# Kernel tuning notes

Measured on AMD Instinct MI355X. Metric: run time of the kernel, lower is better.

## Reference

```python
import jax, jax.numpy as jnp
import numpy as np

D_MODEL = 1024
N_HEADS = 16
D_HEAD = D_MODEL // N_HEADS
BSZ, SEQ = 1, 4096


def setup_inputs() -> dict:
    key = jax.random.key(0)
    ks = jax.random.split(key, 7)
    scale = 1.0 / np.sqrt(D_MODEL)
    q = jax.random.normal(ks[0], (BSZ, SEQ, D_MODEL), dtype=jnp.float32)
    k = jax.random.normal(ks[1], (BSZ, SEQ, D_MODEL), dtype=jnp.float32)
    v = jax.random.normal(ks[2], (BSZ, SEQ, D_MODEL), dtype=jnp.float32)
    Wq = jax.random.normal(ks[3], (D_MODEL, D_MODEL), dtype=jnp.float32) * scale
    Wk = jax.random.normal(ks[4], (D_MODEL, D_MODEL), dtype=jnp.float32) * scale
    Wv = jax.random.normal(ks[5], (D_MODEL, D_MODEL), dtype=jnp.float32) * scale
    Wo = jax.random.normal(ks[6], (D_MODEL, D_MODEL), dtype=jnp.float32) * scale
    # causal mask: 1 = attend, 0 = masked (matches torch masked_fill(mask == 0, -inf))
    mask = jnp.tril(jnp.ones((SEQ, SEQ), dtype=jnp.int32))[None, None, :, :]
    return {"q": q, "k": k, "v": v, "mask": mask, "Wq": Wq, "Wk": Wk, "Wv": Wv, "Wo": Wo}


def reference(q, k, v, mask, Wq, Wk, Wv, Wo):
    bsz, seq, _ = q.shape
    # nn.Linear(d,d,bias=False): y = x @ W.T
    Q = (q @ Wq.T).reshape(bsz, seq, N_HEADS, D_HEAD).transpose(0, 2, 1, 3)
    K = (k @ Wk.T).reshape(bsz, seq, N_HEADS, D_HEAD).transpose(0, 2, 1, 3)
    V = (v @ Wv.T).reshape(bsz, seq, N_HEADS, D_HEAD).transpose(0, 2, 1, 3)
    scores = jnp.einsum("bhqd,bhkd->bhqk", Q, K) / np.sqrt(D_HEAD).astype(np.float32)
    scores = jnp.where(mask == 0, -jnp.inf, scores)
    attn = jax.nn.softmax(scores, axis=-1)
    out = jnp.einsum("bhqk,bhkd->bhqd", attn, V)
    out = out.transpose(0, 2, 1, 3).reshape(bsz, seq, D_MODEL)
    return out @ Wo.T
```

## Files before the change

kernel.cpp:

```cpp
#include <hip/hip_runtime.h>


typedef __attribute__((ext_vector_type(8))) short bf16x8;
typedef __attribute__((ext_vector_type(4))) float f32x4;
typedef __attribute__((ext_vector_type(16))) float f32x16;

#define S_LEN 4096
#define DM 1024
#define NH 16
#define DH 64

static __device__ __forceinline__ unsigned short f2bf(float f) {
  union { float f; unsigned u; } x; x.f = f;
  unsigned u = x.u;
  u += 0x7fffu + ((u >> 16) & 1u);
  return (unsigned short)(u >> 16);
}

static __device__ __forceinline__ unsigned pk2(float lo, float hi) {
  unsigned r;
  asm("v_cvt_pk_bf16_f32 %0, %1, %2" : "=v"(r) : "v"(lo), "v"(hi));
  return r;
}

static __device__ __forceinline__ float exp2_(float x) {
#if __has_builtin(__builtin_amdgcn_exp2f)
  return __builtin_amdgcn_exp2f(x);
#else
  return exp2f(x);
#endif
}

#define GLL16(gsrc, ldst)                                                      \
  __builtin_amdgcn_global_load_lds(                                            \
      (const __attribute__((address_space(1))) void*)(gsrc),                   \
      (__attribute__((address_space(3))) void*)(ldst), 16, 0, 0)

struct CastArgs {
  const float* src[8];
  unsigned short* dst[8];
  int n[8];
  float scl[8];
};

__global__ __launch_bounds__(256) void cast_all(CastArgs a) {
  int which = blockIdx.y;
  const float* __restrict__ src = a.src[which];
  unsigned short* __restrict__ dst = a.dst[which];
  int n = a.n[which];
  float s = a.scl[which];
  int i = (blockIdx.x * 256 + threadIdx.x) * 8;
  if (i >= n) return;
  f32x4 v0 = *(const f32x4*)(src + i);
  f32x4 v1 = *(const f32x4*)(src + i + 4);
  union { bf16x8 v; unsigned short u[8]; } o;
#pragma unroll
  for (int j = 0; j < 4; j++) { o.u[j] = f2bf(v0[j] * s); o.u[4 + j] = f2bf(v1[j] * s); }
  *(bf16x8*)(dst + i) = o.v;
}

static __device__ __forceinline__ void gemm_body(
    const unsigned short* __restrict__ A, const unsigned short* __restrict__ B,
    void* __restrict__ Cout, int mode, unsigned short* As, unsigned short* Bs) {
  const int K = 1024;
  int tid = threadIdx.x;
  int wid = tid >> 6, lane = tid & 63;
  int m0 = blockIdx.y * 128, n0 = blockIdx.x * 128;
  int wr = (wid >> 1) * 64, wc = (wid & 1) * 64;
  int g = lane >> 4, r = lane & 15;

  int lin = wid * 1024 + lane * 16;
  int row0 = lin >> 6;
  int el0 = (lin & 63) >> 1;
  const unsigned short* gA0 = A + (size_t)(m0 + row0) * K + el0;
  const unsigned short* gA1 = gA0 + (size_t)64 * K;
  const unsigned short* gB0 = B + (size_t)(n0 + row0) * K + el0;
  const unsigned short* gB1 = gB0 + (size_t)64 * K;
  unsigned short* lA = As + wid * 512;
  unsigned short* lB = Bs + wid * 512;

  f32x4 acc[4][4] = {};

  for (int k0 = 0; k0 < K; k0 += 32) {
    GLL16(gA0 + k0, lA);
    GLL16(gA1 + k0, lA + 2048);
    GLL16(gB0 + k0, lB);
    GLL16(gB1 + k0, lB + 2048);
    __syncthreads();

    bf16x8 af[4], bfr[4];
#pragma unroll
    for (int mi = 0; mi < 4; mi++)
      af[mi] = *(const bf16x8*)&As[(wr + mi * 16 + r) * 32 + g * 8];
#pragma unroll
    for (int ni = 0; ni < 4; ni++)
      bfr[ni] = *(const bf16x8*)&Bs[(wc + ni * 16 + r) * 32 + g * 8];
#pragma unroll
    for (int mi = 0; mi < 4; mi++)
#pragma unroll
      for (int ni = 0; ni < 4; ni++)
        acc[mi][ni] = __builtin_amdgcn_mfma_f32_16x16x32_bf16(
            af[mi], bfr[ni], acc[mi][ni], 0, 0, 0);
    __syncthreads();
  }

  if (mode == 0) {
    float* C = (float*)Cout;
#pragma unroll
    for (int mi = 0; mi < 4; mi++) {
      int row = m0 + wr + mi * 16 + g * 4;
#pragma unroll
      for (int ni = 0; ni < 4; ni++) {
        int c = n0 + wc + ni * 16 + r;
#pragma unroll
        for (int j = 0; j < 4; j++)
          C[(size_t)(row + j) * DM + c] = acc[mi][ni][j];
      }
    }
  } else if (mode == 1) {
    unsigned short* Cb = (unsigned short*)Cout;
#pragma unroll
    for (int mi = 0; mi < 4; mi++) {
      int row = m0 + wr + mi * 16 + g * 4;
#pragma unroll
      for (int ni = 0; ni < 4; ni++) {
        int c = n0 + wc + ni * 16 + r;
        int h = c >> 6, d = c & 63;
#pragma unroll
        for (int j = 0; j < 4; j++)
          Cb[(size_t)h * (S_LEN * DH) + (size_t)(row + j) * DH + d] =
              f2bf(acc[mi][ni][j]);
      }
    }
  } else {
    unsigned short* Cb = (unsigned short*)Cout;
#pragma unroll
    for (int mi = 0; mi < 4; mi++) {
      int row = m0 + wr + mi * 16 + g * 4;
#pragma unroll
      for (int ni = 0; ni < 4; ni++) {
        int c = n0 + wc + ni * 16 + r;
        int h = c >> 6, d = c & 63;
#pragma unroll
        for (int j = 0; j < 4; j++)
          Cb[(size_t)h * (S_LEN * DH) + (size_t)d * S_LEN + (row + j)] =
              f2bf(acc[mi][ni][j]);
      }
    }
  }
}

struct ProjArgs {
  const unsigned short* A[3];
  const unsigned short* B[3];
  unsigned short* C[3];
  int mode[3];
};

__global__ __launch_bounds__(256, 2) void gemm_proj(ProjArgs p) {
  __shared__ unsigned short As[4096];
  __shared__ unsigned short Bs[4096];
  int z = blockIdx.z;
  gemm_body(p.A[z], p.B[z], p.C[z], p.mode[z], As, Bs);
}

__global__ __launch_bounds__(256, 2) void gemm_one(
    const unsigned short* __restrict__ A, const unsigned short* __restrict__ B,
    void* __restrict__ Cout, int mode) {
  __shared__ unsigned short As[4096];
  __shared__ unsigned short Bs[4096];
  gemm_body(A, B, Cout, mode, As, Bs);
}

__global__ __launch_bounds__(512, 4) void attn_fwd(
    const unsigned short* __restrict__ Qh, const unsigned short* __restrict__ Kh,
    const unsigned short* __restrict__ Vt, unsigned short* __restrict__ O) {
  __shared__ char smem[65536];

  const int b = blockIdx.x;
  const int hd = b & 15;
  const int t = b >> 4;
  const int qe = (t < 16) ? (31 - 2 * t) : (2 * (t - 16));
  const int q0 = qe * 128;
  const int nt = qe + 1;

  const int tid = threadIdx.x;
  const int gg = tid >> 8;
  const int ww = (tid >> 6) & 3;
  const int lane = tid & 63;
  const int l31 = lane & 31, hi = lane >> 5;
  const int qi = ww;
  const int qw = q0 + qi * 32;
  const int qrow = qw + l31;
  const int sw = (l31 & 7) << 4;

  const unsigned short* Qb = Qh + (size_t)hd * (S_LEN * DH);
  const char* Kb = (const char*)(Kh + (size_t)hd * (S_LEN * DH));
  const char* Vb = (const char*)(Vt + (size_t)hd * (S_LEN * DH));

  bf16x8 qf[4];
#pragma unroll
  for (int m = 0; m < 4; m++)
    qf[m] = *(const bf16x8*)&Qb[(size_t)qrow * DH + m * 16 + hi * 8];

  const int roleV = (ww >= 2);
  const int wv = ww & 1;
  const char* gb = roleV ? Vb : Kb;
  const long tstep = roleV ? 128 : 8192;
  int soff[4];
#pragma unroll
  for (int q2 = 0; q2 < 4; q2++) {
    int rowl = wv * 32 + q2 * 8 + (lane >> 3);
    int cb = ((lane & 7) * 16) ^ (((lane >> 3) & 7) << 4);
    soff[q2] = roleV ? (rowl * 8192 + cb) : (rowl * 128 + cb);
  }
  const int ldsc = gg * 32768 + roleV * 8192 + wv * 4096;

  f32x16 oacc[2] = {};
  float m_r = -1e30f, l_r = 0.f;

  {
    const char* gp = gb + (long)(gg * nt) * tstep;
#pragma unroll
    for (int q2 = 0; q2 < 4; q2++)
      GLL16(gp + soff[q2], smem + ldsc + q2 * 1024);
  }
  __syncthreads();

  int db = 0;
  for (int it = 0; it < nt; ++it) {
    if (it + 1 < nt) {
      const char* gp = gb + (long)(gg * nt + it + 1) * tstep;
      char* lb = smem + ldsc + (db ^ 1) * 16384;
#pragma unroll
      for (int q2 = 0; q2 < 4; q2++)
        GLL16(gp + soff[q2], lb + q2 * 1024);
    }
    const int kv0 = (gg * nt + it) * 64;
    const char* Kc = smem + gg * 32768 + db * 16384;
    const char* Vc = Kc + 8192;

    if (kv0 <= qw + 31) {
      const bool hiP = (kv0 + 32 <= qw + 31);
      const bool interior = (kv0 + 63 <= qw);
      f32x16 s0 = {}, s1 = {};
#pragma unroll
      for (int m = 0; m < 4; m++) {
        bf16x8 kf = *(const bf16x8*)(Kc + l31 * 128 + ((m * 32 + hi * 16) ^ sw));
        s0 = __builtin_amdgcn_mfma_f32_32x32x16_bf16(kf, qf[m], s0, 0, 0, 0);
      }
      if (hiP) {
#pragma unroll
        for (int m = 0; m < 4; m++) {
          bf16x8 kf = *(const bf16x8*)(Kc + (32 + l31) * 128 + ((m * 32 + hi * 16) ^ sw));
          s1 = __builtin_amdgcn_mfma_f32_32x32x16_bf16(kf, qf[m], s1, 0, 0, 0);
        }
      }
      if (!interior) {
#pragma unroll
        for (int rg = 0; rg < 16; rg++) {
          const int kvl = (rg & 3) + 8 * (rg >> 2) + 4 * hi;
          s0[rg] = (kv0 + kvl <= qrow) ? s0[rg] : -1e30f;
          s1[rg] = (hiP && kv0 + 32 + kvl <= qrow) ? s1[rg] : -1e30f;
        }
      }
      float a0 = fmaxf(s0[0], s0[1]),  a1 = fmaxf(s0[2], s0[3]);
      float a2 = fmaxf(s0[4], s0[5]),  a3 = fmaxf(s0[6], s0[7]);
      float a4 = fmaxf(s0[8], s0[9]),  a5 = fmaxf(s0[10], s0[11]);
      float a6 = fmaxf(s0[12], s0[13]), a7 = fmaxf(s0[14], s0[15]);
      float b0 = fmaxf(s1[0], s1[1]),  b1 = fmaxf(s1[2], s1[3]);
      float b2 = fmaxf(s1[4], s1[5]),  b3 = fmaxf(s1[6], s1[7]);
      float b4 = fmaxf(s1[8], s1[9]),  b5 = fmaxf(s1[10], s1[11]);
      float b6 = fmaxf(s1[12], s1[13]), b7 = fmaxf(s1[14], s1[15]);
      float c0 = fmaxf(fmaxf(a0, a1), fmaxf(a2, a3));
      float c1 = fmaxf(fmaxf(a4, a5), fmaxf(a6, a7));
      float c2 = fmaxf(fmaxf(b0, b1), fmaxf(b2, b3));
      float c3 = fmaxf(fmaxf(b4, b5), fmaxf(b6, b7));
      float mx = fmaxf(fmaxf(c0, c1), fmaxf(c2, c3));
      mx = fmaxf(mx, __shfl_xor(mx, 32, 64));
      if (__any(mx > m_r + 10.0f)) {
        float mnew = fmaxf(m_r, mx);
        float sc = exp2_(m_r - mnew);
        m_r = mnew;
        l_r *= sc;
#pragma unroll
        for (int dt = 0; dt < 2; dt++)
#pragma unroll
          for (int rg = 0; rg < 16; rg++) oacc[dt][rg] *= sc;
      }
#pragma unroll
      for (int rg = 0; rg < 16; rg++) {
        s0[rg] = exp2_(s0[rg] - m_r);
        s1[rg] = exp2_(s1[rg] - m_r);
      }
      float r0 = (s0[0] + s0[1]) + (s0[2] + s0[3]);
      float r1 = (s0[4] + s0[5]) + (s0[6] + s0[7]);
      float r2 = (s0[8] + s0[9]) + (s0[10] + s0[11]);
      float r3 = (s0[12] + s0[13]) + (s0[14] + s0[15]);
      float r4 = (s1[0] + s1[1]) + (s1[2] + s1[3]);
      float r5 = (s1[4] + s1[5]) + (s1[6] + s1[7]);
      float r6 = (s1[8] + s1[9]) + (s1[10] + s1[11]);
      float r7 = (s1[12] + s1[13]) + (s1[14] + s1[15]);
      float rs = ((r0 + r1) + (r2 + r3)) + ((r4 + r5) + (r6 + r7));
      rs += __shfl_xor(rs, 32, 64);
      l_r += rs;
#pragma unroll
      for (int c = 0; c < 2; c++) {
        if (c == 0 || hiP) {
          const f32x16 P = c ? s1 : s0;
          uint2 pk[4], pp[4];
#pragma unroll
          for (int blk = 0; blk < 4; blk++) {
            pk[blk].x = pk2(P[blk * 4 + 0], P[blk * 4 + 1]);
            pk[blk].y = pk2(P[blk * 4 + 2], P[blk * 4 + 3]);
            pp[blk].x = (unsigned)__shfl_xor((int)pk[blk].x, 32, 64);
            pp[blk].y = (unsigned)__shfl_xor((int)pk[blk].y, 32, 64);
          }
#pragma unroll
          for (int n = 0; n < 2; n++) {
            union { unsigned w[4]; bf16x8 v; } u;
            u.w[0] = hi ? pp[2 * n + 1].x : pk[2 * n].x;
            u.w[1] = hi ? pp[2 * n + 1].y : pk[2 * n].y;
            u.w[2] = hi ? pk[2 * n + 1].x : pp[2 * n].x;
            u.w[3] = hi ? pk[2 * n + 1].y : pp[2 * n].y;
#pragma unroll
            for (int dt = 0; dt < 2; dt++) {
              bf16x8 vf = *(const bf16x8*)(Vc + (dt * 32 + l31) * 128 +
                            ((c * 64 + n * 32 + hi * 16) ^ sw));
              oacc[dt] = __builtin_amdgcn_mfma_f32_32x32x16_bf16(
                  vf, u.v, oacc[dt], 0, 0, 0);
            }
          }
        }
      }
    }
    __syncthreads();
    db ^= 1;
  }

  float* scr = (float*)smem;
  const int sbase = (qi * 64 + lane) * 35;
  if (gg == 1) {
#pragma unroll
    for (int dt = 0; dt < 2; dt++)
#pragma unroll
      for (int rg = 0; rg < 16; rg++) scr[sbase + dt * 16 + rg] = oacc[dt][rg];
    scr[sbase + 32] = m_r;
    scr[sbase + 33] = l_r;
  }
  __syncthreads();
  if (gg == 0) {
    float mB = scr[sbase + 32], lB = scr[sbase + 33];
    float mS = fmaxf(m_r, mB);
    float sA = exp2_(m_r - mS);
    float sB = exp2_(mB - mS);
    float rl = 1.0f / (l_r * sA + lB * sB);
    float fA = sA * rl, fB = sB * rl;
#pragma unroll
    for (int dt = 0; dt < 2; dt++)
#pragma unroll
      for (int blk = 0; blk < 4; blk++) {
        float v0 = oacc[dt][blk * 4 + 0] * fA + scr[sbase + dt * 16 + blk * 4 + 0] * fB;
        float v1 = oacc[dt][blk * 4 + 1] * fA + scr[sbase + dt * 16 + blk * 4 + 1] * fB;
        float v2 = oacc[dt][blk * 4 + 2] * fA + scr[sbase + dt * 16 + blk * 4 + 2] * fB;
        float v3 = oacc[dt][blk * 4 + 3] * fA + scr[sbase + dt * 16 + blk * 4 + 3] * fB;
        uint2 st; st.x = pk2(v0, v1); st.y = pk2(v2, v3);
        int d0 = dt * 32 + blk * 8 + 4 * hi;
        *(uint2*)&O[(size_t)qrow * DM + hd * DH + d0] = st;
      }
  }
}

extern "C" void kernel_launch(void* const* d_in, const int* in_sizes, int n_in,
                              void* d_out, int out_size, void* d_ws, size_t ws_size,
                              hipStream_t stream) {
  const float* q = (const float*)d_in[0];
  const float* k = (const float*)d_in[1];
  const float* v = (const float*)d_in[2];
  const float* Wq = (const float*)d_in[4];
  const float* Wk = (const float*)d_in[5];
  const float* Wv = (const float*)d_in[6];
  const float* Wo = (const float*)d_in[7];

  unsigned short* W = (unsigned short*)d_ws;
  const int SM = S_LEN * DM;
  const int WM = DM * DM;
  unsigned short* qb  = W;
  unsigned short* kb  = qb + SM;
  unsigned short* vb  = kb + SM;
  unsigned short* Wqb = vb + SM;
  unsigned short* Wkb = Wqb + WM;
  unsigned short* Wvb = Wkb + WM;
  unsigned short* Wob = Wvb + WM;
  unsigned short* Qh  = Wob + WM;
  unsigned short* Kh  = Qh + SM;
  unsigned short* Vt  = Kh + SM;
  unsigned short* Ob  = Vt + SM;

  CastArgs ca;
  ca.src[0] = q;  ca.dst[0] = qb;  ca.n[0] = SM; ca.scl[0] = 1.f;
  ca.src[1] = k;  ca.dst[1] = kb;  ca.n[1] = SM; ca.scl[1] = 1.f;
  ca.src[2] = v;  ca.dst[2] = vb;  ca.n[2] = SM; ca.scl[2] = 1.f;
  ca.src[3] = Wq; ca.dst[3] = Wqb; ca.n[3] = WM; ca.scl[3] = 0.125f * 1.44269504f;
  ca.src[4] = Wk; ca.dst[4] = Wkb; ca.n[4] = WM; ca.scl[4] = 1.f;
  ca.src[5] = Wv; ca.dst[5] = Wvb; ca.n[5] = WM; ca.scl[5] = 1.f;
  ca.src[6] = Wo; ca.dst[6] = Wob; ca.n[6] = WM; ca.scl[6] = 1.f;
  ca.src[7] = Wo; ca.dst[7] = Wob; ca.n[7] = 0;  ca.scl[7] = 1.f;
  cast_all<<<dim3(2048, 8), 256, 0, stream>>>(ca);

  ProjArgs pa;
  pa.A[0] = qb; pa.B[0] = Wqb; pa.C[0] = Qh; pa.mode[0] = 1;
  pa.A[1] = kb; pa.B[1] = Wkb; pa.C[1] = Kh; pa.mode[1] = 1;
  pa.A[2] = vb; pa.B[2] = Wvb; pa.C[2] = Vt; pa.mode[2] = 2;
  gemm_proj<<<dim3(8, 32, 3), 256, 0, stream>>>(pa);

  attn_fwd<<<dim3(512), 512, 0, stream>>>(Qh, Kh, Vt, Ob);

  gemm_one<<<dim3(8, 32), 256, 0, stream>>>(Ob, Wob, d_out, 0);
}
```

Before: 142.6 us.

## Restructure attention to direct-global 32-row strips and widen GEMM K tile with swizzle

The attention kernel drops its LDS double-buffered K/V staging. Each block now handles one 32-query strip with two waves splitting the KV range, loading K and a new tiled V layout straight from global memory into registers, and raising MFMA priority with setprio. The V projection output is rewritten into 64x64 tiles to match. The GEMM doubles its K step to 64 and adds an XOR swizzle in LDS to reduce bank conflicts and halve barrier count. The aim is to remove LDS traffic, barriers and the coarse 128-row causal imbalance, at the cost of relying on L2 for K/V reuse across blocks.

```diff
diff --git a/kernel.cpp b/kernel.cpp
--- a/kernel.cpp
+++ b/kernel.cpp
@@ -69,38 +69,43 @@
   int wr = (wid >> 1) * 64, wc = (wid & 1) * 64;
   int g = lane >> 4, r = lane & 15;
 
-  int lin = wid * 1024 + lane * 16;
-  int row0 = lin >> 6;
-  int el0 = (lin & 63) >> 1;
-  const unsigned short* gA0 = A + (size_t)(m0 + row0) * K + el0;
-  const unsigned short* gA1 = gA0 + (size_t)64 * K;
-  const unsigned short* gB0 = B + (size_t)(n0 + row0) * K + el0;
-  const unsigned short* gB1 = gB0 + (size_t)64 * K;
-  unsigned short* lA = As + wid * 512;
-  unsigned short* lB = Bs + wid * 512;
+  const int srow = wid * 8 + (lane >> 3);
+  const int scol = 8 * ((lane & 7) ^ ((lane >> 3) & 7));
+  const unsigned short* gA[4];
+  const unsigned short* gB[4];
+#pragma unroll
+  for (int rr = 0; rr < 4; rr++) {
+    gA[rr] = A + (size_t)(m0 + rr * 32 + srow) * K + scol;
+    gB[rr] = B + (size_t)(n0 + rr * 32 + srow) * K + scol;
+  }
 
   f32x4 acc[4][4] = {};
-
-  for (int k0 = 0; k0 < K; k0 += 32) {
-    GLL16(gA0 + k0, lA);
-    GLL16(gA1 + k0, lA + 2048);
-    GLL16(gB0 + k0, lB);
-    GLL16(gB1 + k0, lB + 2048);
+  const int rsw = (r & 7) << 3;
+
+  for (int k0 = 0; k0 < K; k0 += 64) {
+#pragma unroll
+    for (int rr = 0; rr < 4; rr++) {
+      GLL16(gA[rr] + k0, As + wid * 512 + rr * 2048);
+      GLL16(gB[rr] + k0, Bs + wid * 512 + rr * 2048);
+    }
     __syncthreads();
 
-    bf16x8 af[4], bfr[4];
-#pragma unroll
-    for (int mi = 0; mi < 4; mi++)
-      af[mi] = *(const bf16x8*)&As[(wr + mi * 16 + r) * 32 + g * 8];
-#pragma unroll
-    for (int ni = 0; ni < 4; ni++)
-      bfr[ni] = *(const bf16x8*)&Bs[(wc + ni * 16 + r) * 32 + g * 8];
-#pragma unroll
-    for (int mi = 0; mi < 4; mi++)
+#pragma unroll
+    for (int kk = 0; kk < 64; kk += 32) {
+      bf16x8 af[4], bfr[4];
+#pragma unroll
+      for (int mi = 0; mi < 4; mi++)
+        af[mi] = *(const bf16x8*)&As[(wr + mi * 16 + r) * 64 + ((kk + g * 8) ^ rsw)];
 #pragma unroll
       for (int ni = 0; ni < 4; ni++)
-        acc[mi][ni] = __builtin_amdgcn_mfma_f32_16x16x32_bf16(
-            af[mi], bfr[ni], acc[mi][ni], 0, 0, 0);
+        bfr[ni] = *(const bf16x8*)&Bs[(wc + ni * 16 + r) * 64 + ((kk + g * 8) ^ rsw)];
+#pragma unroll
+      for (int mi = 0; mi < 4; mi++)
+#pragma unroll
+        for (int ni = 0; ni < 4; ni++)
+          acc[mi][ni] = __builtin_amdgcn_mfma_f32_16x16x32_bf16(
+              af[mi], bfr[ni], acc[mi][ni], 0, 0, 0);
+    }
     __syncthreads();
   }
 
@@ -142,9 +147,11 @@
         int c = n0 + wc + ni * 16 + r;
         int h = c >> 6, d = c & 63;
 #pragma unroll
-        for (int j = 0; j < 4; j++)
-          Cb[(size_t)h * (S_LEN * DH) + (size_t)d * S_LEN + (row + j)] =
+        for (int j = 0; j < 4; j++) {
+          int s = row + j;
+          Cb[(size_t)h * (S_LEN * DH) + (size_t)(s >> 6) * 4096 + d * 64 + (s & 63)] =
               f2bf(acc[mi][ni][j]);
+        }
       }
     }
   }
@@ -158,8 +165,8 @@
 };
 
 __global__ __launch_bounds__(256, 2) void gemm_proj(ProjArgs p) {
-  __shared__ unsigned short As[4096];
-  __shared__ unsigned short Bs[4096];
+  __shared__ unsigned short As[8192];
+  __shared__ unsigned short Bs[8192];
   int z = blockIdx.z;
   gemm_body(p.A[z], p.B[z], p.C[z], p.mode[z], As, Bs);
 }
@@ -167,179 +174,152 @@
 __global__ __launch_bounds__(256, 2) void gemm_one(
     const unsigned short* __restrict__ A, const unsigned short* __restrict__ B,
     void* __restrict__ Cout, int mode) {
-  __shared__ unsigned short As[4096];
-  __shared__ unsigned short Bs[4096];
+  __shared__ unsigned short As[8192];
+  __shared__ unsigned short Bs[8192];
   gemm_body(A, B, Cout, mode, As, Bs);
 }
 
-__global__ __launch_bounds__(512, 4) void attn_fwd(
+__global__ __launch_bounds__(128, 3) void attn_fwd(
     const unsigned short* __restrict__ Qh, const unsigned short* __restrict__ Kh,
-    const unsigned short* __restrict__ Vt, unsigned short* __restrict__ O) {
-  __shared__ char smem[65536];
+    const unsigned short* __restrict__ V4, unsigned short* __restrict__ O) {
+  __shared__ float scr[64 * 35];
 
   const int b = blockIdx.x;
   const int hd = b & 15;
-  const int t = b >> 4;
-  const int qe = (t < 16) ? (31 - 2 * t) : (2 * (t - 16));
-  const int q0 = qe * 128;
-  const int nt = qe + 1;
-
+  const int u = b >> 4;
+  const int strip = (u < 64) ? (127 - 2 * u) : (2 * (u - 64));
+  const int qw = strip * 32;
   const int tid = threadIdx.x;
-  const int gg = tid >> 8;
-  const int ww = (tid >> 6) & 3;
+  const int gg = tid >> 6;
   const int lane = tid & 63;
   const int l31 = lane & 31, hi = lane >> 5;
-  const int qi = ww;
-  const int qw = q0 + qi * 32;
   const int qrow = qw + l31;
-  const int sw = (l31 & 7) << 4;
 
   const unsigned short* Qb = Qh + (size_t)hd * (S_LEN * DH);
-  const char* Kb = (const char*)(Kh + (size_t)hd * (S_LEN * DH));
-  const char* Vb = (const char*)(Vt + (size_t)hd * (S_LEN * DH));
+  const unsigned short* Kb = Kh + (size_t)hd * (S_LEN * DH);
+  const unsigned short* Vb = V4 + (size_t)hd * (S_LEN * DH);
 
   bf16x8 qf[4];
 #pragma unroll
   for (int m = 0; m < 4; m++)
     qf[m] = *(const bf16x8*)&Qb[(size_t)qrow * DH + m * 16 + hi * 8];
 
-  const int roleV = (ww >= 2);
-  const int wv = ww & 1;
-  const char* gb = roleV ? Vb : Kb;
-  const long tstep = roleV ? 128 : 8192;
-  int soff[4];
-#pragma unroll
-  for (int q2 = 0; q2 < 4; q2++) {
-    int rowl = wv * 32 + q2 * 8 + (lane >> 3);
-    int cb = ((lane & 7) * 16) ^ (((lane >> 3) & 7) << 4);
-    soff[q2] = roleV ? (rowl * 8192 + cb) : (rowl * 128 + cb);
-  }
-  const int ldsc = gg * 32768 + roleV * 8192 + wv * 4096;
-
   f32x16 oacc[2] = {};
   float m_r = -1e30f, l_r = 0.f;
 
-  {
-    const char* gp = gb + (long)(gg * nt) * tstep;
-#pragma unroll
-    for (int q2 = 0; q2 < 4; q2++)
-      GLL16(gp + soff[q2], smem + ldsc + q2 * 1024);
-  }
-  __syncthreads();
-
-  int db = 0;
-  for (int it = 0; it < nt; ++it) {
-    if (it + 1 < nt) {
-      const char* gp = gb + (long)(gg * nt + it + 1) * tstep;
-      char* lb = smem + ldsc + (db ^ 1) * 16384;
-#pragma unroll
-      for (int q2 = 0; q2 < 4; q2++)
-        GLL16(gp + soff[q2], lb + q2 * 1024);
-    }
-    const int kv0 = (gg * nt + it) * 64;
-    const char* Kc = smem + gg * 32768 + db * 16384;
-    const char* Vc = Kc + 8192;
-
-    if (kv0 <= qw + 31) {
-      const bool hiP = (kv0 + 32 <= qw + 31);
-      const bool interior = (kv0 + 63 <= qw);
-      f32x16 s0 = {}, s1 = {};
-#pragma unroll
-      for (int m = 0; m < 4; m++) {
-        bf16x8 kf = *(const bf16x8*)(Kc + l31 * 128 + ((m * 32 + hi * 16) ^ sw));
-        s0 = __builtin_amdgcn_mfma_f32_32x32x16_bf16(kf, qf[m], s0, 0, 0, 0);
-      }
-      if (hiP) {
-#pragma unroll
-        for (int m = 0; m < 4; m++) {
-          bf16x8 kf = *(const bf16x8*)(Kc + (32 + l31) * 128 + ((m * 32 + hi * 16) ^ sw));
-          s1 = __builtin_amdgcn_mfma_f32_32x32x16_bf16(kf, qf[m], s1, 0, 0, 0);
-        }
-      }
-      if (!interior) {
-#pragma unroll
-        for (int rg = 0; rg < 16; rg++) {
-          const int kvl = (rg & 3) + 8 * (rg >> 2) + 4 * hi;
-          s0[rg] = (kv0 + kvl <= qrow) ? s0[rg] : -1e30f;
-          s1[rg] = (hiP && kv0 + 32 + kvl <= qrow) ? s1[rg] : -1e30f;
-        }
-      }
-      float a0 = fmaxf(s0[0], s0[1]),  a1 = fmaxf(s0[2], s0[3]);
-      float a2 = fmaxf(s0[4], s0[5]),  a3 = fmaxf(s0[6], s0[7]);
-      float a4 = fmaxf(s0[8], s0[9]),  a5 = fmaxf(s0[10], s0[11]);
-      float a6 = fmaxf(s0[12], s0[13]), a7 = fmaxf(s0[14], s0[15]);
-      float b0 = fmaxf(s1[0], s1[1]),  b1 = fmaxf(s1[2], s1[3]);
-      float b2 = fmaxf(s1[4], s1[5]),  b3 = fmaxf(s1[6], s1[7]);
-      float b4 = fmaxf(s1[8], s1[9]),  b5 = fmaxf(s1[10], s1[11]);
-      float b6 = fmaxf(s1[12], s1[13]), b7 = fmaxf(s1[14], s1[15]);
-      float c0 = fmaxf(fmaxf(a0, a1), fmaxf(a2, a3));
-      float c1 = fmaxf(fmaxf(a4, a5), fmaxf(a6, a7));
-      float c2 = fmaxf(fmaxf(b0, b1), fmaxf(b2, b3));
-      float c3 = fmaxf(fmaxf(b4, b5), fmaxf(b6, b7));
-      float mx = fmaxf(fmaxf(c0, c1), fmaxf(c2, c3));
-      mx = fmaxf(mx, __shfl_xor(mx, 32, 64));
-      if (__any(mx > m_r + 10.0f)) {
-        float mnew = fmaxf(m_r, mx);
-        float sc = exp2_(m_r - mnew);
-        m_r = mnew;
-        l_r *= sc;
+  const int nt = (strip >> 1) + 1;
+  const int nh = nt >> 1;
+  const int tb = gg ? nh : 0;
+  const int te = gg ? nt : nh;
+
+  for (int t = tb; t < te; ++t) {
+    const int kv0 = t * 64;
+    const bool hiP = (kv0 + 32 <= qw + 31);
+    const bool diag = (kv0 + 63 > qw);
+    const unsigned short* Kt = Kb + (size_t)kv0 * DH;
+    const unsigned short* Vt = Vb + (size_t)t * 4096;
+
+    bf16x8 kf0[4], kf1[4];
+#pragma unroll
+    for (int m = 0; m < 4; m++)
+      kf0[m] = *(const bf16x8*)&Kt[l31 * DH + m * 16 + hi * 8];
+#pragma unroll
+    for (int m = 0; m < 4; m++)
+      kf1[m] = *(const bf16x8*)&Kt[(32 + l31) * DH + m * 16 + hi * 8];
+    bf16x8 vf[8];
+#pragma unroll
+    for (int i = 0; i < 8; i++) {
+      const int dt = i >> 2, c = (i >> 1) & 1, n = i & 1;
+      vf[i] = *(const bf16x8*)&Vt[(dt * 32 + l31) * 64 + c * 32 + n * 16 + hi * 8];
+    }
+
+    f32x16 s0 = {}, s1 = {};
+    __builtin_amdgcn_s_setprio(1);
+#pragma unroll
+    for (int m = 0; m < 4; m++)
+      s0 = __builtin_amdgcn_mfma_f32_32x32x16_bf16(kf0[m], qf[m], s0, 0, 0, 0);
+#pragma unroll
+    for (int m = 0; m < 4; m++)
+      s1 = __builtin_amdgcn_mfma_f32_32x32x16_bf16(kf1[m], qf[m], s1, 0, 0, 0);
+    __builtin_amdgcn_s_setprio(0);
+
+    if (diag) {
+#pragma unroll
+      for (int rg = 0; rg < 16; rg++) {
+        const int kvl = (rg & 3) + 8 * (rg >> 2) + 4 * hi;
+        s0[rg] = (kv0 + kvl <= qrow) ? s0[rg] : -1e30f;
+        s1[rg] = (hiP && kv0 + 32 + kvl <= qrow) ? s1[rg] : -1e30f;
+      }
+    }
+    float a0 = fmaxf(s0[0], s0[1]),  a1 = fmaxf(s0[2], s0[3]);
+    float a2 = fmaxf(s0[4], s0[5]),  a3 = fmaxf(s0[6], s0[7]);
+    float a4 = fmaxf(s0[8], s0[9]),  a5 = fmaxf(s0[10], s0[11]);
+    float a6 = fmaxf(s0[12], s0[13]), a7 = fmaxf(s0[14], s0[15]);
+    float b0 = fmaxf(s1[0], s1[1]),  b1 = fmaxf(s1[2], s1[3]);
+    float b2 = fmaxf(s1[4], s1[5]),  b3 = fmaxf(s1[6], s1[7]);
+    float b4 = fmaxf(s1[8], s1[9]),  b5 = fmaxf(s1[10], s1[11]);
+    float b6 = fmaxf(s1[12], s1[13]), b7 = fmaxf(s1[14], s1[15]);
+    float c0 = fmaxf(fmaxf(a0, a1), fmaxf(a2, a3));
+    float c1 = fmaxf(fmaxf(a4, a5), fmaxf(a6, a7));
+    float c2 = fmaxf(fmaxf(b0, b1), fmaxf(b2, b3));
+    float c3 = fmaxf(fmaxf(b4, b5), fmaxf(b6, b7));
+    float mx = fmaxf(fmaxf(c0, c1), fmaxf(c2, c3));
+    mx = fmaxf(mx, __shfl_xor(mx, 32, 64));
+    if (__any(mx > m_r + 10.0f)) {
+      float mnew = fmaxf(m_r, mx);
+      float sc = exp2_(m_r - mnew);
+      m_r = mnew;
+      l_r *= sc;
+#pragma unroll
+      for (int dt = 0; dt < 2; dt++)
+#pragma unroll
+        for (int rg = 0; rg < 16; rg++) oacc[dt][rg] *= sc;
+    }
+#pragma unroll
+    for (int rg = 0; rg < 16; rg++) {
+      s0[rg] = exp2_(s0[rg] - m_r);
+      s1[rg] = exp2_(s1[rg] - m_r);
+    }
+    float r0 = (s0[0] + s0[1]) + (s0[2] + s0[3]);
+    float r1 = (s0[4] + s0[5]) + (s0[6] + s0[7]);
+    float r2 = (s0[8] + s0[9]) + (s0[10] + s0[11]);
+    float r3 = (s0[12] + s0[13]) + (s0[14] + s0[15]);
+    float r4 = (s1[0] + s1[1]) + (s1[2] + s1[3]);
+    float r5 = (s1[4] + s1[5]) + (s1[6] + s1[7]);
+    float r6 = (s1[8] + s1[9]) + (s1[10] + s1[11]);
+    float r7 = (s1[12] + s1[13]) + (s1[14] + s1[15]);
+    float rs = ((r0 + r1) + (r2 + r3)) + ((r4 + r5) + (r6 + r7));
+    rs += __shfl_xor(rs, 32, 64);
+    l_r += rs;
+#pragma unroll
+    for (int c = 0; c < 2; c++) {
+      const f32x16 P = c ? s1 : s0;
+      uint2 pk[4], pp[4];
+#pragma unroll
+      for (int blk = 0; blk < 4; blk++) {
+        pk[blk].x = pk2(P[blk * 4 + 0], P[blk * 4 + 1]);
+        pk[blk].y = pk2(P[blk * 4 + 2], P[blk * 4 + 3]);
+        pp[blk].x = (unsigned)__shfl_xor((int)pk[blk].x, 32, 64);
+        pp[blk].y = (unsigned)__shfl_xor((int)pk[blk].y, 32, 64);
+      }
+      __builtin_amdgcn_s_setprio(1);
+#pragma unroll
+      for (int n = 0; n < 2; n++) {
+        union { unsigned w[4]; bf16x8 v; } u2;
+        u2.w[0] = hi ? pp[2 * n + 1].x : pk[2 * n].x;
+        u2.w[1] = hi ? pp[2 * n + 1].y : pk[2 * n].y;
+        u2.w[2] = hi ? pk[2 * n + 1].x : pp[2 * n].x;
+        u2.w[3] = hi ? pk[2 * n + 1].y : pp[2 * n].y;
 #pragma unroll
         for (int dt = 0; dt < 2; dt++)
-#pragma unroll
-          for (int rg = 0; rg < 16; rg++) oacc[dt][rg] *= sc;
-      }
-#pragma unroll
-      for (int rg = 0; rg < 16; rg++) {
-        s0[rg] = exp2_(s0[rg] - m_r);
-        s1[rg] = exp2_(s1[rg] - m_r);
-      }
-      float r0 = (s0[0] + s0[1]) + (s0[2] + s0[3]);
-      float r1 = (s0[4] + s0[5]) + (s0[6] + s0[7]);
-      float r2 = (s0[8] + s0[9]) + (s0[10] + s0[11]);
-      float r3 = (s0[12] + s0[13]) + (s0[14] + s0[15]);
-      float r4 = (s1[0] + s1[1]) + (s1[2] + s1[3]);
-      float r5 = (s1[4] + s1[5]) + (s1[6] + s1[7]);
-      float r6 = (s1[8] + s1[9]) + (s1[10] + s1[11]);
-      float r7 = (s1[12] + s1[13]) + (s1[14] + s1[15]);
-      float rs = ((r0 + r1) + (r2 + r3)) + ((r4 + r5) + (r6 + r7));
-      rs += __shfl_xor(rs, 32, 64);
-      l_r += rs;
-#pragma unroll
-      for (int c = 0; c < 2; c++) {
-        if (c == 0 || hiP) {
-          const f32x16 P = c ? s1 : s0;
-          uint2 pk[4], pp[4];
-#pragma unroll
-          for (int blk = 0; blk < 4; blk++) {
-            pk[blk].x = pk2(P[blk * 4 + 0], P[blk * 4 + 1]);
-            pk[blk].y = pk2(P[blk * 4 + 2], P[blk * 4 + 3]);
-            pp[blk].x = (unsigned)__shfl_xor((int)pk[blk].x, 32, 64);
-            pp[blk].y = (unsigned)__shfl_xor((int)pk[blk].y, 32, 64);
-          }
-#pragma unroll
-          for (int n = 0; n < 2; n++) {
-            union { unsigned w[4]; bf16x8 v; } u;
-            u.w[0] = hi ? pp[2 * n + 1].x : pk[2 * n].x;
-            u.w[1] = hi ? pp[2 * n + 1].y : pk[2 * n].y;
-            u.w[2] = hi ? pk[2 * n + 1].x : pp[2 * n].x;
-            u.w[3] = hi ? pk[2 * n + 1].y : pp[2 * n].y;
-#pragma unroll
-            for (int dt = 0; dt < 2; dt++) {
-              bf16x8 vf = *(const bf16x8*)(Vc + (dt * 32 + l31) * 128 +
-                            ((c * 64 + n * 32 + hi * 16) ^ sw));
-              oacc[dt] = __builtin_amdgcn_mfma_f32_32x32x16_bf16(
-                  vf, u.v, oacc[dt], 0, 0, 0);
-            }
-          }
-        }
-      }
-    }
-    __syncthreads();
-    db ^= 1;
-  }
-
-  float* scr = (float*)smem;
-  const int sbase = (qi * 64 + lane) * 35;
+          oacc[dt] = __builtin_amdgcn_mfma_f32_32x32x16_bf16(
+              vf[dt * 4 + c * 2 + n], u2.v, oacc[dt], 0, 0, 0);
+      }
+      __builtin_amdgcn_s_setprio(0);
+    }
+  }
+
+  const int sbase = lane * 35;
   if (gg == 1) {
 #pragma unroll
     for (int dt = 0; dt < 2; dt++)
@@ -394,8 +374,8 @@
   unsigned short* Wob = Wvb + WM;
   unsigned short* Qh  = Wob + WM;
   unsigned short* Kh  = Qh + SM;
-  unsigned short* Vt  = Kh + SM;
-  unsigned short* Ob  = Vt + SM;
+  unsigned short* V4  = Kh + SM;
+  unsigned short* Ob  = V4 + SM;
 
   CastArgs ca;
   ca.src[0] = q;  ca.dst[0] = qb;  ca.n[0] = SM; ca.scl[0] = 1.f;
@@ -411,10 +391,10 @@
   ProjArgs pa;
   pa.A[0] = qb; pa.B[0] = Wqb; pa.C[0] = Qh; pa.mode[0] = 1;
   pa.A[1] = kb; pa.B[1] = Wkb; pa.C[1] = Kh; pa.mode[1] = 1;
-  pa.A[2] = vb; pa.B[2] = Wvb; pa.C[2] = Vt; pa.mode[2] = 2;
+  pa.A[2] = vb; pa.B[2] = Wvb; pa.C[2] = V4; pa.mode[2] = 2;
   gemm_proj<<<dim3(8, 32, 3), 256, 0, stream>>>(pa);
 
-  attn_fwd<<<dim3(512), 512, 0, stream>>>(Qh, Kh, Vt, Ob);
+  attn_fwd<<<dim3(2048), 128, 0, stream>>>(Qh, Kh, V4, Ob);
 
   gemm_one<<<dim3(8, 32), 256, 0, stream>>>(Ob, Wob, d_out, 0);
 }
```

Result: slower. 216.8 us (+52.0%).

## Use BK=64 swizzled GEMM tiles and a tiled V layout for contiguous attention loads

Applied to the files above, without the earlier changes.

The GEMM K-step grows from 32 to 64. Shared tiles are XOR-swizzled so that LDS fragment reads avoid bank conflicts, and each stage now has half as many barriers. The V projection is written in 64-row blocks, each stored as [d][s&63], so attention loads a V tile as one contiguous 8 KB chunk like K, replacing the strided 128-byte rows. The softmax max reduction is also regrouped into 3-input fmax, which costs more LDS per GEMM block and may lower occupancy.

```diff
diff --git a/kernel.cpp b/kernel.cpp
--- a/kernel.cpp
+++ b/kernel.cpp
@@ -69,38 +69,43 @@
   int wr = (wid >> 1) * 64, wc = (wid & 1) * 64;
   int g = lane >> 4, r = lane & 15;
 
-  int lin = wid * 1024 + lane * 16;
-  int row0 = lin >> 6;
-  int el0 = (lin & 63) >> 1;
-  const unsigned short* gA0 = A + (size_t)(m0 + row0) * K + el0;
-  const unsigned short* gA1 = gA0 + (size_t)64 * K;
-  const unsigned short* gB0 = B + (size_t)(n0 + row0) * K + el0;
-  const unsigned short* gB1 = gB0 + (size_t)64 * K;
-  unsigned short* lA = As + wid * 512;
-  unsigned short* lB = Bs + wid * 512;
+  const int srow = wid * 8 + (lane >> 3);
+  const int scol = 8 * ((lane & 7) ^ ((lane >> 3) & 7));
+  const unsigned short* gA[4];
+  const unsigned short* gB[4];
+#pragma unroll
+  for (int rr = 0; rr < 4; rr++) {
+    gA[rr] = A + (size_t)(m0 + rr * 32 + srow) * K + scol;
+    gB[rr] = B + (size_t)(n0 + rr * 32 + srow) * K + scol;
+  }
 
   f32x4 acc[4][4] = {};
-
-  for (int k0 = 0; k0 < K; k0 += 32) {
-    GLL16(gA0 + k0, lA);
-    GLL16(gA1 + k0, lA + 2048);
-    GLL16(gB0 + k0, lB);
-    GLL16(gB1 + k0, lB + 2048);
+  const int rsw = (r & 7) << 3;
+
+  for (int k0 = 0; k0 < K; k0 += 64) {
+#pragma unroll
+    for (int rr = 0; rr < 4; rr++) {
+      GLL16(gA[rr] + k0, As + wid * 512 + rr * 2048);
+      GLL16(gB[rr] + k0, Bs + wid * 512 + rr * 2048);
+    }
     __syncthreads();
 
-    bf16x8 af[4], bfr[4];
-#pragma unroll
-    for (int mi = 0; mi < 4; mi++)
-      af[mi] = *(const bf16x8*)&As[(wr + mi * 16 + r) * 32 + g * 8];
-#pragma unroll
-    for (int ni = 0; ni < 4; ni++)
-      bfr[ni] = *(const bf16x8*)&Bs[(wc + ni * 16 + r) * 32 + g * 8];
-#pragma unroll
-    for (int mi = 0; mi < 4; mi++)
+#pragma unroll
+    for (int kk = 0; kk < 64; kk += 32) {
+      bf16x8 af[4], bfr[4];
+#pragma unroll
+      for (int mi = 0; mi < 4; mi++)
+        af[mi] = *(const bf16x8*)&As[(wr + mi * 16 + r) * 64 + ((kk + g * 8) ^ rsw)];
 #pragma unroll
       for (int ni = 0; ni < 4; ni++)
-        acc[mi][ni] = __builtin_amdgcn_mfma_f32_16x16x32_bf16(
-            af[mi], bfr[ni], acc[mi][ni], 0, 0, 0);
+        bfr[ni] = *(const bf16x8*)&Bs[(wc + ni * 16 + r) * 64 + ((kk + g * 8) ^ rsw)];
+#pragma unroll
+      for (int mi = 0; mi < 4; mi++)
+#pragma unroll
+        for (int ni = 0; ni < 4; ni++)
+          acc[mi][ni] = __builtin_amdgcn_mfma_f32_16x16x32_bf16(
+              af[mi], bfr[ni], acc[mi][ni], 0, 0, 0);
+    }
     __syncthreads();
   }
 
@@ -142,9 +147,11 @@
         int c = n0 + wc + ni * 16 + r;
         int h = c >> 6, d = c & 63;
 #pragma unroll
-        for (int j = 0; j < 4; j++)
-          Cb[(size_t)h * (S_LEN * DH) + (size_t)d * S_LEN + (row + j)] =
+        for (int j = 0; j < 4; j++) {
+          int s = row + j;
+          Cb[(size_t)h * (S_LEN * DH) + (size_t)(s >> 6) * 4096 + d * 64 + (s & 63)] =
               f2bf(acc[mi][ni][j]);
+        }
       }
     }
   }
@@ -158,8 +165,8 @@
 };
 
 __global__ __launch_bounds__(256, 2) void gemm_proj(ProjArgs p) {
-  __shared__ unsigned short As[4096];
-  __shared__ unsigned short Bs[4096];
+  __shared__ unsigned short As[8192];
+  __shared__ unsigned short Bs[8192];
   int z = blockIdx.z;
   gemm_body(p.A[z], p.B[z], p.C[z], p.mode[z], As, Bs);
 }
@@ -167,14 +174,14 @@
 __global__ __launch_bounds__(256, 2) void gemm_one(
     const unsigned short* __restrict__ A, const unsigned short* __restrict__ B,
     void* __restrict__ Cout, int mode) {
-  __shared__ unsigned short As[4096];
-  __shared__ unsigned short Bs[4096];
+  __shared__ unsigned short As[8192];
+  __shared__ unsigned short Bs[8192];
   gemm_body(A, B, Cout, mode, As, Bs);
 }
 
 __global__ __launch_bounds__(512, 4) void attn_fwd(
     const unsigned short* __restrict__ Qh, const unsigned short* __restrict__ Kh,
-    const unsigned short* __restrict__ Vt, unsigned short* __restrict__ O) {
+    const unsigned short* __restrict__ V4, unsigned short* __restrict__ O) {
   __shared__ char smem[65536];
 
   const int b = blockIdx.x;
@@ -196,7 +203,7 @@
 
   const unsigned short* Qb = Qh + (size_t)hd * (S_LEN * DH);
   const char* Kb = (const char*)(Kh + (size_t)hd * (S_LEN * DH));
-  const char* Vb = (const char*)(Vt + (size_t)hd * (S_LEN * DH));
+  const char* Vb = (const char*)(V4 + (size_t)hd * (S_LEN * DH));
 
   bf16x8 qf[4];
 #pragma unroll
@@ -206,13 +213,12 @@
   const int roleV = (ww >= 2);
   const int wv = ww & 1;
   const char* gb = roleV ? Vb : Kb;
-  const long tstep = roleV ? 128 : 8192;
   int soff[4];
 #pragma unroll
   for (int q2 = 0; q2 < 4; q2++) {
     int rowl = wv * 32 + q2 * 8 + (lane >> 3);
     int cb = ((lane & 7) * 16) ^ (((lane >> 3) & 7) << 4);
-    soff[q2] = roleV ? (rowl * 8192 + cb) : (rowl * 128 + cb);
+    soff[q2] = rowl * 128 + cb;
   }
   const int ldsc = gg * 32768 + roleV * 8192 + wv * 4096;
 
@@ -220,7 +226,7 @@
   float m_r = -1e30f, l_r = 0.f;
 
   {
-    const char* gp = gb + (long)(gg * nt) * tstep;
+    const char* gp = gb + (long)(gg * nt) * 8192;
 #pragma unroll
     for (int q2 = 0; q2 < 4; q2++)
       GLL16(gp + soff[q2], smem + ldsc + q2 * 1024);
@@ -230,7 +236,7 @@
   int db = 0;
   for (int it = 0; it < nt; ++it) {
     if (it + 1 < nt) {
-      const char* gp = gb + (long)(gg * nt + it + 1) * tstep;
+      const char* gp = gb + (long)(gg * nt + it + 1) * 8192;
       char* lb = smem + ldsc + (db ^ 1) * 16384;
 #pragma unroll
       for (int q2 = 0; q2 < 4; q2++)
@@ -264,19 +270,22 @@
           s1[rg] = (hiP && kv0 + 32 + kvl <= qrow) ? s1[rg] : -1e30f;
         }
       }
-      float a0 = fmaxf(s0[0], s0[1]),  a1 = fmaxf(s0[2], s0[3]);
-      float a2 = fmaxf(s0[4], s0[5]),  a3 = fmaxf(s0[6], s0[7]);
-      float a4 = fmaxf(s0[8], s0[9]),  a5 = fmaxf(s0[10], s0[11]);
-      float a6 = fmaxf(s0[12], s0[13]), a7 = fmaxf(s0[14], s0[15]);
-      float b0 = fmaxf(s1[0], s1[1]),  b1 = fmaxf(s1[2], s1[3]);
-      float b2 = fmaxf(s1[4], s1[5]),  b3 = fmaxf(s1[6], s1[7]);
-      float b4 = fmaxf(s1[8], s1[9]),  b5 = fmaxf(s1[10], s1[11]);
-      float b6 = fmaxf(s1[12], s1[13]), b7 = fmaxf(s1[14], s1[15]);
-      float c0 = fmaxf(fmaxf(a0, a1), fmaxf(a2, a3));
-      float c1 = fmaxf(fmaxf(a4, a5), fmaxf(a6, a7));
-      float c2 = fmaxf(fmaxf(b0, b1), fmaxf(b2, b3));
-      float c3 = fmaxf(fmaxf(b4, b5), fmaxf(b6, b7));
-      float mx = fmaxf(fmaxf(c0, c1), fmaxf(c2, c3));
+      float t0 = fmaxf(fmaxf(s0[0], s0[1]), s0[2]);
+      float t1 = fmaxf(fmaxf(s0[3], s0[4]), s0[5]);
+      float t2 = fmaxf(fmaxf(s0[6], s0[7]), s0[8]);
+      float t3 = fmaxf(fmaxf(s0[9], s0[10]), s0[11]);
+      float t4 = fmaxf(fmaxf(s0[12], s0[13]), s0[14]);
+      float t5 = fmaxf(fmaxf(s0[15], s1[0]), s1[1]);
+      float t6 = fmaxf(fmaxf(s1[2], s1[3]), s1[4]);
+      float t7 = fmaxf(fmaxf(s1[5], s1[6]), s1[7]);
+      float t8 = fmaxf(fmaxf(s1[8], s1[9]), s1[10]);
+      float t9 = fmaxf(fmaxf(s1[11], s1[12]), s1[13]);
+      float ta = fmaxf(s1[14], s1[15]);
+      float u0 = fmaxf(fmaxf(t0, t1), t2);
+      float u1 = fmaxf(fmaxf(t3, t4), t5);
+      float u2 = fmaxf(fmaxf(t6, t7), t8);
+      float u3 = fmaxf(t9, ta);
+      float mx = fmaxf(fmaxf(u0, u1), fmaxf(u2, u3));
       mx = fmaxf(mx, __shfl_xor(mx, 32, 64));
       if (__any(mx > m_r + 10.0f)) {
         float mnew = fmaxf(m_r, mx);
@@ -394,8 +403,8 @@
   unsigned short* Wob = Wvb + WM;
   unsigned short* Qh  = Wob + WM;
   unsigned short* Kh  = Qh + SM;
-  unsigned short* Vt  = Kh + SM;
-  unsigned short* Ob  = Vt + SM;
+  unsigned short* V4  = Kh + SM;
+  unsigned short* Ob  = V4 + SM;
 
   CastArgs ca;
   ca.src[0] = q;  ca.dst[0] = qb;  ca.n[0] = SM; ca.scl[0] = 1.f;
@@ -411,10 +420,10 @@
   ProjArgs pa;
   pa.A[0] = qb; pa.B[0] = Wqb; pa.C[0] = Qh; pa.mode[0] = 1;
   pa.A[1] = kb; pa.B[1] = Wkb; pa.C[1] = Kh; pa.mode[1] = 1;
-  pa.A[2] = vb; pa.B[2] = Wvb; pa.C[2] = Vt; pa.mode[2] = 2;
+  pa.A[2] = vb; pa.B[2] = Wvb; pa.C[2] = V4; pa.mode[2] = 2;
   gemm_proj<<<dim3(8, 32, 3), 256, 0, stream>>>(pa);
 
-  attn_fwd<<<dim3(512), 512, 0, stream>>>(Qh, Kh, Vt, Ob);
+  attn_fwd<<<dim3(512), 512, 0, stream>>>(Qh, Kh, V4, Ob);
 
   gemm_one<<<dim3(8, 32), 256, 0, stream>>>(Ob, Wob, d_out, 0);
 }
```

New measurement: 133.5 us. 6.4% less time.
